# Optimization experiments

Measured on AMD Instinct MI355X. Metric: run time of the kernel, lower is better.

The kernel has to match this reference:

```python
import jax, jax.numpy as jnp
import numpy as np

B, S, HIDDEN, N_HEADS = 1, 2048, 2048, 16
HEAD_DIM = HIDDEN // N_HEADS  # 128


def setup_inputs() -> dict:
    key = jax.random.key(0)
    ks = jax.random.split(key, 7)
    w = 0.02  # init scale for projection weights
    return {
        "x_self": jax.random.normal(ks[0], (B, S, HIDDEN), jnp.float32),
        "x_cross": jax.random.normal(ks[1], (B, S, HIDDEN), jnp.float32),
        "mask": jnp.zeros((B, 1, S, S), jnp.float32),
        "Wq": jax.random.normal(ks[2], (HIDDEN, HIDDEN), jnp.float32) * w,
        "Wk": jax.random.normal(ks[3], (HIDDEN, HIDDEN), jnp.float32) * w,
        "Wv": jax.random.normal(ks[4], (HIDDEN, HIDDEN), jnp.float32) * w,
        "Wo": jax.random.normal(ks[5], (HIDDEN, HIDDEN), jnp.float32) * w,
    }


def reference(x_self, x_cross, mask, Wq, Wk, Wv, Wo):
    bf16 = jnp.bfloat16
    b = x_self.shape[0]
    scale = HEAD_DIM ** -0.5

    def split_heads(x):  # [b, s, hidden] -> [b, h, s, d]
        return x.reshape(b, -1, N_HEADS, HEAD_DIM).transpose(0, 2, 1, 3)

    # projections run in bf16 (weights cast to bf16 in the original)
    q_self = split_heads((x_self.astype(bf16) @ Wq.astype(bf16).T))
    q_cross = split_heads((x_cross.astype(bf16) @ Wq.astype(bf16).T))
    # k/v for both self and cross blocks come from x_self with identical weights
    k = split_heads((x_self.astype(bf16) @ Wk.astype(bf16).T))
    v = split_heads((x_self.astype(bf16) @ Wv.astype(bf16).T))

    def attn_block(qh):
        # fp32 upcast for QK^T + softmax, then bf16 cast for AV (dropout p=0 -> identity)
        w = jnp.einsum('bhqd,bhkd->bhqk', qh.astype(jnp.float32), k.astype(jnp.float32)) * scale
        w = w + mask
        w = jax.nn.softmax(w, axis=-1).astype(bf16)
        return jnp.einsum('bhqk,bhkd->bhqd', w, v.astype(bf16))  # [b, h, s, d] bf16

    out_self = attn_block(q_self)
    out_cross = attn_block(q_cross)
    out = jnp.concatenate([out_self, out_cross], axis=1)          # [b, 2h, s, d]
    out_flat = out.transpose(0, 2, 1, 3).reshape(b, -1, HIDDEN)   # [b, 2s, hidden]
    Wo_bf = Wo.astype(bf16)
    out_final = 0.5 * (out_flat @ Wo_bf.T + out_flat @ Wo_bf.T)
    return out_final.astype(jnp.float32)
```

## Files before the change

kernel.cpp:

```cpp
#include <hip/hip_runtime.h>
#include <hip/hip_bf16.h>
#include <stdint.h>

#define S 2048
#define HID 2048
#define NH 16
#define HD 128

typedef short short8 __attribute__((ext_vector_type(8)));
typedef float f32x4 __attribute__((ext_vector_type(4)));
typedef float f32x16 __attribute__((ext_vector_type(16)));
typedef uint32_t u32;
typedef u32 u32x4 __attribute__((ext_vector_type(4)));

__device__ __forceinline__ ushort f2bf(float x) {
  uint32_t u = __builtin_bit_cast(uint32_t, x);
  if ((u & 0x7fffffffu) > 0x7f800000u) return (ushort)((u >> 16) | 0x40);
  uint32_t r = u + 0x7fffu + ((u >> 16) & 1u);
  return (ushort)(r >> 16);
}
__device__ __forceinline__ float bf2f(ushort u) {
  union { uint32_t i; float f; } c; c.i = ((uint32_t)u) << 16; return c.f;
}

__device__ __forceinline__ void glds16(const ushort* g, ushort* l) {
  __builtin_amdgcn_global_load_lds((const __attribute__((address_space(1))) uint32_t*)g,
                                   (__attribute__((address_space(3))) uint32_t*)l, 16, 0, 0);
}

__device__ __forceinline__ void mfma16(f32x4& d, short8 a, short8 b) {
  asm("v_mfma_f32_16x16x32_bf16 %0, %1, %2, %0" : "+v"(d) : "v"(a), "v"(b));
}
__device__ __forceinline__ void mfma32(f32x16& d, short8 a, short8 b) {
  asm("v_mfma_f32_32x32x16_bf16 %0, %1, %2, %0" : "+v"(d) : "v"(a), "v"(b));
}
__device__ __forceinline__ void plswap(u32& a, u32& b) {
  asm("v_permlane32_swap_b32 %0, %1" : "+v"(a), "+v"(b));
}
__device__ __forceinline__ u32 cvtpk(float lo, float hi) {
  u32 r; asm("v_cvt_pk_bf16_f32 %0, %1, %2" : "=v"(r) : "v"(lo), "v"(hi)); return r;
}

__global__ __launch_bounds__(256) void cast_f32_bf16_k(const float* __restrict__ in,
                                                       ushort* __restrict__ out, int n4) {
  int i = blockIdx.x * 256 + threadIdx.x;
  if (i >= n4) return;
  float4 v = ((const float4*)in)[i];
  ushort4 o;
  o.x = f2bf(v.x); o.y = f2bf(v.y); o.z = f2bf(v.z); o.w = f2bf(v.w);
  ((ushort4*)out)[i] = o;
}

template <int OUTF32, int NSPLIT>
__global__ __launch_bounds__(256)
void gemm_bt_k(const ushort* __restrict__ A, const ushort* __restrict__ B,
               void* __restrict__ C, int M, int N, int K) {
  __shared__ __align__(16) ushort ldsA[128 * 64];
  __shared__ __align__(16) ushort ldsB[128 * 64];
  const int tid = threadIdx.x, lane = tid & 63, wid = tid >> 6;
  const int g = lane >> 4, c = lane & 15;
  const int wr = wid >> 1, wc = wid & 1;
  const long m0 = (long)blockIdx.y * 128, n0 = (long)blockIdx.x * 128;
  const int srow = lane >> 3, sslot = lane & 7;

  f32x4 acc[4][4] = {};

  for (int k0 = 0; k0 < K; k0 += 64) {
#pragma unroll
    for (int i = 0; i < 4; ++i) {
      int ii = wid * 4 + i;
      int rt = ii * 8 + srow;
      int col = ((sslot ^ (rt & 7)) << 3) + k0;
      glds16(A + (m0 + rt) * (long)K + col, ldsA + ii * 512);
      glds16(B + (n0 + rt) * (long)K + col, ldsB + ii * 512);
    }
    __syncthreads();
#pragma unroll
    for (int kk = 0; kk < 2; ++kk) {
      short8 af[4], bfr[4];
#pragma unroll
      for (int m = 0; m < 4; ++m) {
        int row = wr * 64 + m * 16 + c;
        af[m] = *(const short8*)(ldsA + row * 64 + (((kk * 4 + g) ^ (row & 7)) << 3));
      }
#pragma unroll
      for (int n = 0; n < 4; ++n) {
        int row = wc * 64 + n * 16 + c;
        bfr[n] = *(const short8*)(ldsB + row * 64 + (((kk * 4 + g) ^ (row & 7)) << 3));
      }
#pragma unroll
      for (int m = 0; m < 4; ++m)
#pragma unroll
        for (int n = 0; n < 4; ++n) mfma16(acc[m][n], af[m], bfr[n]);
    }
    __syncthreads();
  }
  asm volatile("s_nop 7\n\ts_nop 7");
#pragma unroll
  for (int m = 0; m < 4; ++m) {
#pragma unroll
    for (int r = 0; r < 4; ++r) {
      long grow = m0 + wr * 64 + m * 16 + g * 4 + r;
#pragma unroll
      for (int n = 0; n < 4; ++n) {
        long gcol = n0 + wc * 64 + n * 16 + c;
        long idx;
        if (NSPLIT) idx = ((gcol >> 11) << 22) + (grow << 11) + (gcol & 2047);
        else        idx = grow * N + gcol;
        float v = acc[m][n][r];
        if (OUTF32) ((float*)C)[idx] = bf2f(f2bf(v));
        else        ((ushort*)C)[idx] = f2bf(v);
      }
    }
  }
}

__global__ __launch_bounds__(256)
void transpose_bf16_k(const ushort* __restrict__ in, ushort* __restrict__ out) {
  __shared__ __align__(16) ushort t[64][72];
  const int tid = threadIdx.x;
  const long bx = (long)blockIdx.x * 64;
  const long by = (long)blockIdx.y * 64;
#pragma unroll
  for (int i = 0; i < 2; ++i) {
    int row = (tid >> 3) + i * 32;
    int col = (tid & 7) * 8;
    *(short8*)(&t[row][col]) = *(const short8*)(in + (by + row) * 2048 + bx + col);
  }
  __syncthreads();
#pragma unroll
  for (int i = 0; i < 2; ++i) {
    int orow = (tid >> 3) + i * 32;
    int ocol = (tid & 7) * 8;
    short8 v;
#pragma unroll
    for (int j = 0; j < 8; ++j) v[j] = (short)t[ocol + j][orow];
    *(short8*)(out + (bx + orow) * 2048 + by + ocol) = v;
  }
}

__global__ __launch_bounds__(512)
void attn2_k(const ushort* __restrict__ Qself, const ushort* __restrict__ Qcross,
             const ushort* __restrict__ Kp, const ushort* __restrict__ Vt,
             const float* __restrict__ mask, ushort* __restrict__ outf) {
  __shared__ __align__(16) ushort ldsK[64 * 128];
  __shared__ __align__(16) ushort ldsV[128 * 64];
  const int tid = threadIdx.x, lane = tid & 63, wid = tid >> 6;
  const int c31 = lane & 31, hi = lane >> 5;
  const int h = blockIdx.y, blk = blockIdx.z;
  const ushort* Qp = blk ? Qcross : Qself;
  const int qbase = blockIdx.x * 256 + wid * 32;
  const long qme = qbase + c31;

  short8 qf[8];
#pragma unroll
  for (int ks = 0; ks < 8; ++ks)
    qf[ks] = *(const short8*)(Qp + qme * HID + h * HD + ks * 16 + hi * 8);

  f32x16 o[4] = {};
  float m_r = -__builtin_inff(), l_r = 0.f;

  const float SL = 0.08838834764831845f * 1.4426950408889634f;
  const float ML = 1.4426950408889634f;

  const int kRow4 = lane >> 4, kSlot = lane & 15;
  const int vRow8 = lane >> 3, vSlot = lane & 7;

  for (int kv0 = 0; kv0 < S; kv0 += 64) {
#pragma unroll
    for (int i = 0; i < 2; ++i) {
      int seg = i * 8 + wid;
      int rk = seg * 4 + kRow4;
      glds16(Kp + (long)(kv0 + rk) * HID + h * HD + ((kSlot ^ (rk & 15)) << 3),
             ldsK + seg * 512);
      int rv = seg * 8 + vRow8;
      glds16(Vt + (long)(h * HD + rv) * S + kv0 + ((vSlot ^ (rv & 7)) << 3),
             ldsV + seg * 512);
    }
    __syncthreads();

    f32x4 mv[2][4];
#pragma unroll
    for (int kvb = 0; kvb < 2; ++kvb)
#pragma unroll
      for (int rg = 0; rg < 4; ++rg)
        mv[kvb][rg] = *(const f32x4*)(mask + qme * S + kv0 + kvb * 32 + rg * 8 + hi * 4);

    f32x16 s0 = {}, s1 = {};
#pragma unroll
    for (int ks = 0; ks < 8; ++ks) {
      int r0 = c31, r1 = 32 + c31;
      short8 kf0 = *(const short8*)(ldsK + r0 * 128 + (((ks * 2 + hi) ^ (r0 & 15)) << 3));
      short8 kf1 = *(const short8*)(ldsK + r1 * 128 + (((ks * 2 + hi) ^ (r1 & 15)) << 3));
      mfma32(s0, kf0, qf[ks]);
      mfma32(s1, kf1, qf[ks]);
    }
    asm volatile("s_nop 7\n\ts_nop 7");

#pragma unroll
    for (int r = 0; r < 16; ++r) {
      s0[r] = s0[r] * SL + mv[0][r >> 2][r & 3] * ML;
      s1[r] = s1[r] * SL + mv[1][r >> 2][r & 3] * ML;
    }

    float pmax = s0[0];
#pragma unroll
    for (int r = 1; r < 16; ++r) pmax = fmaxf(pmax, s0[r]);
#pragma unroll
    for (int r = 0; r < 16; ++r) pmax = fmaxf(pmax, s1[r]);
    pmax = fmaxf(pmax, __shfl_xor(pmax, 32));

    if (!__all(pmax <= m_r + 8.f)) {
      float mnew = fmaxf(m_r, pmax);
      float alpha = __builtin_amdgcn_exp2f(m_r - mnew);
      m_r = mnew;
      l_r *= alpha;
#pragma unroll
      for (int r = 0; r < 16; ++r) {
        float alf = __shfl(alpha, (r & 3) + 8 * (r >> 2) + 4 * hi);
#pragma unroll
        for (int dt = 0; dt < 4; ++dt) o[dt][r] *= alf;
      }
    }

    float lsum = 0.f;
#pragma unroll
    for (int r = 0; r < 16; ++r) {
      s0[r] = __builtin_amdgcn_exp2f(s0[r] - m_r); lsum += s0[r];
      s1[r] = __builtin_amdgcn_exp2f(s1[r] - m_r); lsum += s1[r];
    }
    lsum += __shfl_xor(lsum, 32);
    l_r += lsum;

    short8 pa[4];
#pragma unroll
    for (int kk = 0; kk < 4; ++kk) {
      const f32x16& sv = (kk < 2) ? s0 : s1;
      const int b = (kk & 1) * 8;
      u32 x0 = cvtpk(sv[b + 0], sv[b + 1]);
      u32 x1 = cvtpk(sv[b + 2], sv[b + 3]);
      u32 y0 = cvtpk(sv[b + 4], sv[b + 5]);
      u32 y1 = cvtpk(sv[b + 6], sv[b + 7]);
      plswap(x0, y0);
      plswap(x1, y1);
      u32x4 t; t[0] = x0; t[1] = x1; t[2] = y0; t[3] = y1;
      pa[kk] = __builtin_bit_cast(short8, t);
    }
    asm volatile("s_nop 3");

#pragma unroll
    for (int dt = 0; dt < 4; ++dt) {
      int row = dt * 32 + c31;
#pragma unroll
      for (int kk = 0; kk < 4; ++kk) {
        short8 vf = *(const short8*)(ldsV + row * 64 + (((kk * 2 + hi) ^ (row & 7)) << 3));
        mfma32(o[dt], pa[kk], vf);
      }
    }
    __syncthreads();
  }

  asm volatile("s_nop 7\n\ts_nop 7");
#pragma unroll
  for (int r = 0; r < 16; ++r) {
    int qr = (r & 3) + 8 * (r >> 2) + 4 * hi;
    float linv = 1.0f / __shfl(l_r, qr);
    long orow = 2L * (qbase + qr) + blk;
#pragma unroll
    for (int dt = 0; dt < 4; ++dt)
      outf[orow * HID + h * HD + dt * 32 + c31] = f2bf(o[dt][r] * linv);
  }
}

extern "C" void kernel_launch(void* const* d_in, const int* in_sizes, int n_in,
                              void* d_out, int out_size, void* d_ws, size_t ws_size,
                              hipStream_t stream) {
  (void)in_sizes; (void)n_in; (void)out_size; (void)ws_size;
  const float* x_self  = (const float*)d_in[0];
  const float* x_cross = (const float*)d_in[1];
  const float* mask    = (const float*)d_in[2];
  const float* Wq      = (const float*)d_in[3];
  const float* Wk      = (const float*)d_in[4];
  const float* Wv      = (const float*)d_in[5];
  const float* Wo      = (const float*)d_in[6];

  uint8_t* w = (uint8_t*)d_ws;
  const size_t MB8 = (size_t)S * HID * sizeof(ushort);
  ushort* xs_bf   = (ushort*)(w + 0 * MB8);
  ushort* xc_bf   = (ushort*)(w + 1 * MB8);
  ushort* Wq_bf   = (ushort*)(w + 2 * MB8);
  ushort* Wk_bf   = (ushort*)(w + 3 * MB8);
  ushort* Wv_bf   = (ushort*)(w + 4 * MB8);
  ushort* Wo_bf   = (ushort*)(w + 5 * MB8);
  ushort* q_self  = (ushort*)(w + 6 * MB8);
  ushort* q_cross = (ushort*)(w + 7 * MB8);
  ushort* k_      = (ushort*)(w + 8 * MB8);
  ushort* v_      = (ushort*)(w + 9 * MB8);
  ushort* vt       = xs_bf;
  ushort* out_flat = Wq_bf;

  const int n4 = S * HID / 4;
  dim3 cg((n4 + 255) / 256);
  cast_f32_bf16_k<<<cg, 256, 0, stream>>>(x_self,  xs_bf, n4);
  cast_f32_bf16_k<<<cg, 256, 0, stream>>>(x_cross, xc_bf, n4);
  cast_f32_bf16_k<<<cg, 256, 0, stream>>>(Wq, Wq_bf, n4);
  cast_f32_bf16_k<<<cg, 256, 0, stream>>>(Wk, Wk_bf, n4);
  cast_f32_bf16_k<<<cg, 256, 0, stream>>>(Wv, Wv_bf, n4);
  cast_f32_bf16_k<<<cg, 256, 0, stream>>>(Wo, Wo_bf, n4);

  gemm_bt_k<0, 0><<<dim3(16, 32), 256, 0, stream>>>(xs_bf, Wq_bf, q_self, 4096, 2048, 2048);
  gemm_bt_k<0, 1><<<dim3(32, 16), 256, 0, stream>>>(xs_bf, Wk_bf, k_, 2048, 4096, 2048);

  transpose_bf16_k<<<dim3(32, 32), 256, 0, stream>>>(v_, vt);

  attn2_k<<<dim3(8, 16, 2), 512, 0, stream>>>(q_self, q_cross, k_, vt, mask, out_flat);

  gemm_bt_k<1, 0><<<dim3(16, 32), 256, 0, stream>>>(out_flat, Wo_bf, d_out, 4096, 2048, 2048);
}
```

Measured before the change: 275.1 us.

## Double-buffer K/V tiles in attention and merge six cast launches into one

The attention kernel now uses two LDS buffers for K and V. The next tile is prefetched with global_load_lds while the current tile is computed, so only one barrier is needed per iteration. MFMA sections are wrapped in s_setprio raises, the scale/log2e handling is restructured (same rescale threshold in natural units), and the six separate f32->bf16 cast launches become one batched launch over a 2D grid. This doubles LDS use per block, which may reduce occupancy, in exchange for hiding load latency and launch overhead.

Measured after the change: 265.5 us. 1.04x faster.

```diff
diff --git a/kernel.cpp b/kernel.cpp
--- a/kernel.cpp
+++ b/kernel.cpp
@@ -41,10 +41,11 @@
   u32 r; asm("v_cvt_pk_bf16_f32 %0, %1, %2" : "=v"(r) : "v"(lo), "v"(hi)); return r;
 }
 
-__global__ __launch_bounds__(256) void cast_f32_bf16_k(const float* __restrict__ in,
-                                                       ushort* __restrict__ out, int n4) {
+struct CastArgs { const float* s[6]; ushort* d[6]; };
+__global__ __launch_bounds__(256) void cast6_k(CastArgs a) {
+  const float* in = a.s[blockIdx.y];
+  ushort* out = a.d[blockIdx.y];
   int i = blockIdx.x * 256 + threadIdx.x;
-  if (i >= n4) return;
   float4 v = ((const float4*)in)[i];
   ushort4 o;
   o.x = f2bf(v.x); o.y = f2bf(v.y); o.z = f2bf(v.z); o.w = f2bf(v.w);
@@ -140,11 +141,11 @@
 }
 
 __global__ __launch_bounds__(512)
-void attn2_k(const ushort* __restrict__ Qself, const ushort* __restrict__ Qcross,
+void attn3_k(const ushort* __restrict__ Qself, const ushort* __restrict__ Qcross,
              const ushort* __restrict__ Kp, const ushort* __restrict__ Vt,
              const float* __restrict__ mask, ushort* __restrict__ outf) {
-  __shared__ __align__(16) ushort ldsK[64 * 128];
-  __shared__ __align__(16) ushort ldsV[128 * 64];
+  __shared__ __align__(16) ushort ldsK[2 * 64 * 128];
+  __shared__ __align__(16) ushort ldsV[2 * 128 * 64];
   const int tid = threadIdx.x, lane = tid & 63, wid = tid >> 6;
   const int c31 = lane & 31, hi = lane >> 5;
   const int h = blockIdx.y, blk = blockIdx.z;
@@ -160,47 +161,61 @@
   f32x16 o[4] = {};
   float m_r = -__builtin_inff(), l_r = 0.f;
 
-  const float SL = 0.08838834764831845f * 1.4426950408889634f;
-  const float ML = 1.4426950408889634f;
+  const float SC  = 0.08838834764831845f;
+  const float L2E = 1.4426950408889634f;
+  const float THR = 5.545177444479562f;
 
   const int kRow4 = lane >> 4, kSlot = lane & 15;
   const int vRow8 = lane >> 3, vSlot = lane & 7;
-
-  for (int kv0 = 0; kv0 < S; kv0 += 64) {
-#pragma unroll
-    for (int i = 0; i < 2; ++i) {
-      int seg = i * 8 + wid;
-      int rk = seg * 4 + kRow4;
-      glds16(Kp + (long)(kv0 + rk) * HID + h * HD + ((kSlot ^ (rk & 15)) << 3),
-             ldsK + seg * 512);
-      int rv = seg * 8 + vRow8;
-      glds16(Vt + (long)(h * HD + rv) * S + kv0 + ((vSlot ^ (rv & 7)) << 3),
-             ldsV + seg * 512);
-    }
-    __syncthreads();
+  const float* mrow = mask + qme * (long)S;
+
+#define STAGE(BO, KV0) do {                                                       \
+    _Pragma("unroll")                                                             \
+    for (int i_ = 0; i_ < 2; ++i_) {                                              \
+      int seg = i_ * 8 + wid;                                                     \
+      int rk = seg * 4 + kRow4;                                                   \
+      glds16(Kp + (long)((KV0) + rk) * HID + h * HD + ((kSlot ^ (rk & 15)) << 3), \
+             ldsK + (BO) * 8192 + seg * 512);                                     \
+      int rv = seg * 8 + vRow8;                                                   \
+      glds16(Vt + (long)(h * HD + rv) * S + (KV0) + ((vSlot ^ (rv & 7)) << 3),    \
+             ldsV + (BO) * 8192 + seg * 512);                                     \
+    }                                                                             \
+  } while (0)
+
+  STAGE(0, 0);
+  __syncthreads();
+
+  for (int t = 0; t < 32; ++t) {
+    const int bo = t & 1;
+    const ushort* kb = ldsK + bo * 8192;
+    const ushort* vb = ldsV + bo * 8192;
+    if (t < 31) STAGE(bo ^ 1, (t + 1) * 64);
+    const int kv0 = t * 64;
 
     f32x4 mv[2][4];
 #pragma unroll
     for (int kvb = 0; kvb < 2; ++kvb)
 #pragma unroll
       for (int rg = 0; rg < 4; ++rg)
-        mv[kvb][rg] = *(const f32x4*)(mask + qme * S + kv0 + kvb * 32 + rg * 8 + hi * 4);
+        mv[kvb][rg] = *(const f32x4*)(mrow + kv0 + kvb * 32 + rg * 8 + hi * 4);
 
     f32x16 s0 = {}, s1 = {};
+    __builtin_amdgcn_s_setprio(1);
 #pragma unroll
     for (int ks = 0; ks < 8; ++ks) {
       int r0 = c31, r1 = 32 + c31;
-      short8 kf0 = *(const short8*)(ldsK + r0 * 128 + (((ks * 2 + hi) ^ (r0 & 15)) << 3));
-      short8 kf1 = *(const short8*)(ldsK + r1 * 128 + (((ks * 2 + hi) ^ (r1 & 15)) << 3));
+      short8 kf0 = *(const short8*)(kb + r0 * 128 + (((ks * 2 + hi) ^ (r0 & 15)) << 3));
+      short8 kf1 = *(const short8*)(kb + r1 * 128 + (((ks * 2 + hi) ^ (r1 & 15)) << 3));
       mfma32(s0, kf0, qf[ks]);
       mfma32(s1, kf1, qf[ks]);
     }
+    __builtin_amdgcn_s_setprio(0);
     asm volatile("s_nop 7\n\ts_nop 7");
 
 #pragma unroll
     for (int r = 0; r < 16; ++r) {
-      s0[r] = s0[r] * SL + mv[0][r >> 2][r & 3] * ML;
-      s1[r] = s1[r] * SL + mv[1][r >> 2][r & 3] * ML;
+      s0[r] = __builtin_fmaf(s0[r], SC, mv[0][r >> 2][r & 3]);
+      s1[r] = __builtin_fmaf(s1[r], SC, mv[1][r >> 2][r & 3]);
     }
 
     float pmax = s0[0];
@@ -210,9 +225,9 @@
     for (int r = 0; r < 16; ++r) pmax = fmaxf(pmax, s1[r]);
     pmax = fmaxf(pmax, __shfl_xor(pmax, 32));
 
-    if (!__all(pmax <= m_r + 8.f)) {
+    if (!__all(pmax <= m_r + THR)) {
       float mnew = fmaxf(m_r, pmax);
-      float alpha = __builtin_amdgcn_exp2f(m_r - mnew);
+      float alpha = __builtin_amdgcn_exp2f((m_r - mnew) * L2E);
       m_r = mnew;
       l_r *= alpha;
 #pragma unroll
@@ -223,11 +238,12 @@
       }
     }
 
+    const float nm = -m_r * L2E;
     float lsum = 0.f;
 #pragma unroll
     for (int r = 0; r < 16; ++r) {
-      s0[r] = __builtin_amdgcn_exp2f(s0[r] - m_r); lsum += s0[r];
-      s1[r] = __builtin_amdgcn_exp2f(s1[r] - m_r); lsum += s1[r];
+      s0[r] = __builtin_amdgcn_exp2f(__builtin_fmaf(s0[r], L2E, nm)); lsum += s0[r];
+      s1[r] = __builtin_amdgcn_exp2f(__builtin_fmaf(s1[r], L2E, nm)); lsum += s1[r];
     }
     lsum += __shfl_xor(lsum, 32);
     l_r += lsum;
@@ -243,22 +259,26 @@
       u32 y1 = cvtpk(sv[b + 6], sv[b + 7]);
       plswap(x0, y0);
       plswap(x1, y1);
-      u32x4 t; t[0] = x0; t[1] = x1; t[2] = y0; t[3] = y1;
-      pa[kk] = __builtin_bit_cast(short8, t);
+      u32x4 tt; tt[0] = x0; tt[1] = x1; tt[2] = y0; tt[3] = y1;
+      pa[kk] = __builtin_bit_cast(short8, tt);
     }
     asm volatile("s_nop 3");
 
+    __builtin_amdgcn_s_setprio(1);
 #pragma unroll
     for (int dt = 0; dt < 4; ++dt) {
       int row = dt * 32 + c31;
 #pragma unroll
       for (int kk = 0; kk < 4; ++kk) {
-        short8 vf = *(const short8*)(ldsV + row * 64 + (((kk * 2 + hi) ^ (row & 7)) << 3));
+        short8 vf = *(const short8*)(vb + row * 64 + (((kk * 2 + hi) ^ (row & 7)) << 3));
         mfma32(o[dt], pa[kk], vf);
       }
     }
+    __builtin_amdgcn_s_setprio(0);
+
     __syncthreads();
   }
+#undef STAGE
 
   asm volatile("s_nop 7\n\ts_nop 7");
 #pragma unroll
@@ -299,21 +319,21 @@
   ushort* vt       = xs_bf;
   ushort* out_flat = Wq_bf;
 
-  const int n4 = S * HID / 4;
-  dim3 cg((n4 + 255) / 256);
-  cast_f32_bf16_k<<<cg, 256, 0, stream>>>(x_self,  xs_bf, n4);
-  cast_f32_bf16_k<<<cg, 256, 0, stream>>>(x_cross, xc_bf, n4);
-  cast_f32_bf16_k<<<cg, 256, 0, stream>>>(Wq, Wq_bf, n4);
-  cast_f32_bf16_k<<<cg, 256, 0, stream>>>(Wk, Wk_bf, n4);
-  cast_f32_bf16_k<<<cg, 256, 0, stream>>>(Wv, Wv_bf, n4);
-  cast_f32_bf16_k<<<cg, 256, 0, stream>>>(Wo, Wo_bf, n4);
+  CastArgs ca;
+  ca.s[0] = x_self;  ca.d[0] = xs_bf;
+  ca.s[1] = x_cross; ca.d[1] = xc_bf;
+  ca.s[2] = Wq;      ca.d[2] = Wq_bf;
+  ca.s[3] = Wk;      ca.d[3] = Wk_bf;
+  ca.s[4] = Wv;      ca.d[4] = Wv_bf;
+  ca.s[5] = Wo;      ca.d[5] = Wo_bf;
+  cast6_k<<<dim3(4096, 6), 256, 0, stream>>>(ca);
 
   gemm_bt_k<0, 0><<<dim3(16, 32), 256, 0, stream>>>(xs_bf, Wq_bf, q_self, 4096, 2048, 2048);
   gemm_bt_k<0, 1><<<dim3(32, 16), 256, 0, stream>>>(xs_bf, Wk_bf, k_, 2048, 4096, 2048);
 
   transpose_bf16_k<<<dim3(32, 32), 256, 0, stream>>>(v_, vt);
 
-  attn2_k<<<dim3(8, 16, 2), 512, 0, stream>>>(q_self, q_cross, k_, vt, mask, out_flat);
+  attn3_k<<<dim3(8, 16, 2), 512, 0, stream>>>(q_self, q_cross, k_, vt, mask, out_flat);
 
   gemm_bt_k<1, 0><<<dim3(16, 32), 256, 0, stream>>>(out_flat, Wo_bf, d_out, 4096, 2048, 2048);
 }
```
